# Kernel tuning notes

Hardware: AMD Instinct MI355X
Metric: run time of the kernel (lower is better)

The kernel has to match this reference:

```python
import jax, jax.numpy as jnp
import numpy as np

B, F, N, NO = 1, 512, 8192, 21
L1, L2, L3 = 640, 256, 128


def setup_inputs() -> dict:
    key = jax.random.key(0)
    ks = jax.random.split(key, 32)
    rn = lambda k, s: jax.random.normal(k, s, dtype=jnp.float32)
    inp = {
        "emb1": rn(ks[0], (B, F, N)),
        "emb2": rn(ks[1], (B, F, N)),
        "t1": rn(ks[2], (B, 3, N)),
        "t2": rn(ks[3], (B, 3, N)),
        "obj": jax.random.randint(ks[4], (B, 1), 0, NO, dtype=jnp.int32),
    }
    # 1x1 Conv1d weights == dense (out,in) matrices + bias
    dims_r = [(L1, 2 * F), (L2, L1), (L3, L2), (NO * 4, L3)]
    dims_t = [(L1, 2 * F), (L2, L1), (L3, L2), (NO * 3, L3)]
    ki = 5
    for br, dims in (("r", dims_r), ("t", dims_t)):
        for i, (o, c) in enumerate(dims, start=1):
            inp[f"w{i}{br}"] = rn(ks[ki], (o, c)) * (1.0 / np.sqrt(c)); ki += 1
            inp[f"b{i}{br}"] = rn(ks[ki], (o,)) * 0.01; ki += 1
    return inp


def _knn1(ref, qry):
    # ref, qry: (3, N). For each query point j, index of nearest ref point.
    g = ref.T @ qry  # (N_ref, N_qry)
    d2 = jnp.sum(ref * ref, axis=0)[:, None] + jnp.sum(qry * qry, axis=0)[None, :] - 2.0 * g
    return jnp.argmin(d2, axis=0)  # (N_qry,)


def _branch(x, w1, b1, w2, b2, w3, b3, w4, b4):
    h = jax.nn.relu(w1 @ x + b1[:, None])
    h = jax.nn.relu(w2 @ h + b2[:, None])
    h = jax.nn.relu(w3 @ h + b3[:, None])
    return w4 @ h + b4[:, None]


def reference(emb1, emb2, t1, t2, obj,
              w1r, b1r, w2r, b2r, w3r, b3r, w4r, b4r,
              w1t, b1t, w2t, b2t, w3t, b3t, w4t, b4t):
    bs, num_feat, num_points = emb1.shape
    t1 = t1.reshape(bs, 3, -1)
    t2 = t2.reshape(bs, 3, -1)
    # brute-force 1-NN of each t2 point among t1 points (bs == 1)
    idx = _knn1(t1[0], t2[0])  # (N,) zero-based (torch code subtracts 1 from 1-based inds)
    emb1g = emb1[0][:, idx]  # gather matched features, (F, N)
    # torch.stack([emb1,emb2],dim=1).view(bs, 2F, N) == channel concat [emb1g; emb2]
    emb = jnp.concatenate([emb1g, emb2[0]], axis=0)  # (2F, N)
    rx = _branch(emb, w1r, b1r, w2r, b2r, w3r, b3r, w4r, b4r).reshape(NO, 4, num_points)
    tx = _branch(emb, w1t, b1t, w2t, b2t, w3t, b3t, w4t, b4t).reshape(NO, 3, num_points)
    obj0 = obj[0]  # (1,)
    out_rx = jnp.transpose(rx[obj0], (0, 2, 1))  # (1, N, 4)
    out_tx = jnp.transpose(tx[obj0], (0, 2, 1))  # (1, N, 3)
    return out_rx, out_tx
```

## Files before the change

kernel.cpp:

```cpp
#include <hip/hip_runtime.h>

typedef unsigned short u16;
typedef __bf16 bf16x8 __attribute__((ext_vector_type(8)));
typedef float f32x4 __attribute__((ext_vector_type(4)));

__device__ __forceinline__ float b2f(u16 v) {
    return __uint_as_float(((unsigned int)v) << 16);
}
__device__ __forceinline__ u16 f2b(float f) {
    unsigned int u = __float_as_uint(f);
    u += 0x7fffu + ((u >> 16) & 1u);
    return (u16)(u >> 16);
}

__device__ __forceinline__ void ld_lds16(const u16* g, u16* l) {
    __builtin_amdgcn_global_load_lds(
        (__attribute__((address_space(1))) void*)(uintptr_t)(const void*)g,
        (__attribute__((address_space(3))) void*)l, 16, 0, 0);
}

__global__ void pack_w_k(const float* __restrict__ w1r, const float* __restrict__ w1t,
                         const float* __restrict__ w2r, const float* __restrict__ w2t,
                         const float* __restrict__ w3r, const float* __restrict__ w3t,
                         u16* __restrict__ dst)
{
    size_t i = (size_t)blockIdx.x * 2048 + (size_t)threadIdx.x * 8;
    const float* src; size_t off;
    if (i < 655360)       { src = w1r; off = 0; }
    else if (i < 1310720) { src = w1t; off = 655360; }
    else if (i < 1474560) { src = w2r; off = 1310720; }
    else if (i < 1638400) { src = w2t; off = 1474560; }
    else if (i < 1671168) { src = w3r; off = 1638400; }
    else                  { src = w3t; off = 1671168; }
    const float4 lo = *(const float4*)(src + (i - off));
    const float4 hi = *(const float4*)(src + (i - off) + 4);
    ushort4 o0, o1;
    o0.x = f2b(lo.x); o0.y = f2b(lo.y); o0.z = f2b(lo.z); o0.w = f2b(lo.w);
    o1.x = f2b(hi.x); o1.y = f2b(hi.y); o1.z = f2b(hi.z); o1.w = f2b(hi.w);
    *(ushort4*)(dst + i) = o0;
    *(ushort4*)(dst + i + 4) = o1;
}

__global__ void knn_k(const float* __restrict__ t1, const float* __restrict__ t2,
                      unsigned long long* __restrict__ keys)
{
    __shared__ float4 ref[128];
    const int t = threadIdx.x;
    const int rs = blockIdx.x;
    const int qb = blockIdx.y;
    if (t < 128) {
        int i = rs * 128 + t;
        float x = t1[i], y = t1[8192 + i], z = t1[16384 + i];
        float rr = __fadd_rn(__fadd_rn(__fmul_rn(x, x), __fmul_rn(y, y)), __fmul_rn(z, z));
        ref[t] = make_float4(x, y, z, rr);
    }
    __syncthreads();

    float qx[8], qy[8], qz[8], qq[8], bestd[8];
    int besti[8];
    const int q0 = qb * 2048 + t;
#pragma unroll
    for (int j = 0; j < 8; ++j) {
        int q = q0 + j * 256;
        qx[j] = t2[q]; qy[j] = t2[8192 + q]; qz[j] = t2[16384 + q];
        qq[j] = __fadd_rn(__fadd_rn(__fmul_rn(qx[j], qx[j]), __fmul_rn(qy[j], qy[j])),
                          __fmul_rn(qz[j], qz[j]));
        bestd[j] = __uint_as_float(0x7f800000u);
        besti[j] = 0;
    }
    for (int i = 0; i < 128; ++i) {
        float4 r = ref[i];
        int ridx = rs * 128 + i;
#pragma unroll
        for (int j = 0; j < 8; ++j) {
            float g = __fmaf_rn(qz[j], r.z, __fmaf_rn(qy[j], r.y, __fmul_rn(qx[j], r.x)));
            float d2 = __fsub_rn(__fadd_rn(r.w, qq[j]), __fmul_rn(2.0f, g));
            if (d2 < bestd[j]) { bestd[j] = d2; besti[j] = ridx; }
        }
    }
#pragma unroll
    for (int j = 0; j < 8; ++j) {
        unsigned long long key =
            ((unsigned long long)__float_as_uint(bestd[j]) << 32) | (unsigned int)besti[j];
        atomicMin(&keys[q0 + j * 256], key);
    }
}

__global__ void transpose_k(const float* __restrict__ e1, const float* __restrict__ e2,
                            u16* __restrict__ o1, u16* __restrict__ o2)
{
    __shared__ float tile[64][65];
    const float* in = blockIdx.z ? e2 : e1;
    u16* out = blockIdx.z ? o2 : o1;
    const int ostride = blockIdx.z ? 1024 : 512;
    const int coff = blockIdx.z ? 512 : 0;
    const int t = threadIdx.x;
    const int n0 = blockIdx.x * 64, f0 = blockIdx.y * 64;
    const int c = t & 63, r4 = t >> 6;
#pragma unroll
    for (int p = 0; p < 16; ++p) {
        int fr = p * 4 + r4;
        tile[fr][c] = in[(size_t)(f0 + fr) * 8192 + n0 + c];
    }
    __syncthreads();
    const int fc = (t & 15) * 4;
    const int nr4 = t >> 4;
#pragma unroll
    for (int p = 0; p < 4; ++p) {
        int nr = p * 16 + nr4;
        ushort4 o;
        o.x = f2b(tile[fc + 0][nr]); o.y = f2b(tile[fc + 1][nr]);
        o.z = f2b(tile[fc + 2][nr]); o.w = f2b(tile[fc + 3][nr]);
        *(ushort4*)&out[(size_t)(n0 + nr) * ostride + coff + f0 + fc] = o;
    }
}

__global__ void gather_k(const unsigned long long* __restrict__ keys,
                         const u16* __restrict__ emb1t, u16* __restrict__ Xt)
{
    const int t = threadIdx.x, w = t >> 6, l = t & 63;
    const int nbase = blockIdx.x * 32;
#pragma unroll
    for (int it = 0; it < 8; ++it) {
        int n = nbase + it * 4 + w;
        int i = (int)(keys[n] & 0xffffffffu);
        const uint4* src = (const uint4*)(emb1t + (size_t)i * 512);
        uint4* dst = (uint4*)(Xt + (size_t)n * 1024);
        dst[l] = src[l];
    }
}

template <int TN>
__global__ __launch_bounds__(256) void gemm_bt(
    const u16* __restrict__ Ar, const u16* __restrict__ At,
    const float* __restrict__ biasr, const float* __restrict__ biast,
    const u16* __restrict__ Bt, u16* __restrict__ Ct,
    int Mh, int K, int bstride, int b_step, int ostride, int relu)
{
    constexpr int NJ = TN / 32;
    __shared__ __align__(16) u16 lds_a[128 * 32];
    __shared__ __align__(16) u16 lds_b[TN * 32];

    const int t = threadIdx.x;
    const int n0 = blockIdx.x * TN;
    const int m0 = blockIdx.y * 128;
    const int branch = blockIdx.z;

    const u16* A = branch ? At : Ar;
    const float* bias = branch ? biast : biasr;
    const int b_off = branch * b_step;
    const int out_off = branch * Mh;

    const int w = t >> 6, l = t & 63;
    const int sr = l >> 2, sc = (l & 3) * 8;

    const u16* gA0 = A + (size_t)(m0 + w * 32 + sr) * K + sc;
    const u16* gA1 = gA0 + (size_t)16 * K;
    u16* lA0 = &lds_a[w * 1024];
    u16* lA1 = lA0 + 512;

    const u16* gB0;
    const u16* gB1 = nullptr;
    u16 *lB0, *lB1 = nullptr;
    if (TN == 128) {
        gB0 = Bt + (size_t)(n0 + w * 32 + sr) * bstride + b_off + sc;
        gB1 = gB0 + (size_t)16 * bstride;
        lB0 = &lds_b[w * 1024];
        lB1 = lB0 + 512;
    } else {
        gB0 = Bt + (size_t)(n0 + w * 16 + sr) * bstride + b_off + sc;
        lB0 = &lds_b[w * 512];
    }

    const int wm = (w & 1) * 64;
    const int wn = (w >> 1) * (TN / 2);
    const int lrow = l & 15, quad = l >> 4;
    const u16* fa = &lds_a[(wm + lrow) * 32 + quad * 8];
    const u16* fb = &lds_b[(wn + lrow) * 32 + quad * 8];

    f32x4 acc[4][NJ];
#pragma unroll
    for (int i = 0; i < 4; ++i)
#pragma unroll
        for (int j = 0; j < NJ; ++j)
            acc[i][j] = (f32x4){0.f, 0.f, 0.f, 0.f};

    ld_lds16(gA0, lA0); ld_lds16(gA1, lA1);
    ld_lds16(gB0, lB0);
    if (TN == 128) ld_lds16(gB1, lB1);

    for (int kt = 0; kt < K; kt += 32) {
        __syncthreads();
        bf16x8 af[4], bfr[NJ];
#pragma unroll
        for (int i = 0; i < 4; ++i) af[i] = *(const bf16x8*)(fa + i * 16 * 32);
#pragma unroll
        for (int j = 0; j < NJ; ++j) bfr[j] = *(const bf16x8*)(fb + j * 16 * 32);
        __syncthreads();
        if (kt + 32 < K) {
            gA0 += 32; gA1 += 32; gB0 += 32;
            ld_lds16(gA0, lA0); ld_lds16(gA1, lA1);
            ld_lds16(gB0, lB0);
            if (TN == 128) { gB1 += 32; ld_lds16(gB1, lB1); }
        }
#pragma unroll
        for (int i = 0; i < 4; ++i)
#pragma unroll
            for (int j = 0; j < NJ; ++j)
                acc[i][j] = __builtin_amdgcn_mfma_f32_16x16x32_bf16(
                    af[i], bfr[j], acc[i][j], 0, 0, 0);
    }

#pragma unroll
    for (int i = 0; i < 4; ++i) {
        const int mbase = m0 + wm + i * 16 + quad * 4;
        const float4 bbv = *(const float4*)&bias[mbase];
#pragma unroll
        for (int j = 0; j < NJ; ++j) {
            const int n = n0 + wn + j * 16 + lrow;
            f32x4 v = acc[i][j];
            float x0 = v[0] + bbv.x, x1 = v[1] + bbv.y;
            float x2 = v[2] + bbv.z, x3 = v[3] + bbv.w;
            if (relu) {
                x0 = fmaxf(x0, 0.f); x1 = fmaxf(x1, 0.f);
                x2 = fmaxf(x2, 0.f); x3 = fmaxf(x3, 0.f);
            }
            ushort4 o;
            o.x = f2b(x0); o.y = f2b(x1); o.z = f2b(x2); o.w = f2b(x3);
            *(ushort4*)&Ct[(size_t)n * ostride + out_off + mbase] = o;
        }
    }
}

__global__ __launch_bounds__(256) void gemm3_final_k(
    const u16* __restrict__ Ar, const u16* __restrict__ At,
    const float* __restrict__ b3r, const float* __restrict__ b3t,
    const u16* __restrict__ Bt,
    const float* __restrict__ w4r, const float* __restrict__ b4r,
    const float* __restrict__ w4t, const float* __restrict__ b4t,
    const int* __restrict__ objp, float* __restrict__ out)
{
    __shared__ __align__(16) u16 lds_a[128 * 32];
    __shared__ __align__(16) u16 lds_b[64 * 32];
    __shared__ __align__(16) float lds_h[64 * 132];
    __shared__ __align__(16) float lds_w[4 * 132];

    const int t = threadIdx.x;
    const int n0 = blockIdx.x * 64;
    const int branch = blockIdx.y;

    const u16* A = branch ? At : Ar;
    const float* bias = branch ? b3t : b3r;
    const int b_off = branch * 256;

    const int w = t >> 6, l = t & 63;
    const int sr = l >> 2, sc = (l & 3) * 8;

    const u16* gA0 = A + (size_t)(w * 32 + sr) * 256 + sc;
    const u16* gA1 = gA0 + (size_t)16 * 256;
    u16* lA0 = &lds_a[w * 1024];
    u16* lA1 = lA0 + 512;

    const u16* gB0 = Bt + (size_t)(n0 + w * 16 + sr) * 512 + b_off + sc;
    u16* lB0 = &lds_b[w * 512];

    const int wm = (w & 1) * 64;
    const int wn = (w >> 1) * 32;
    const int lrow = l & 15, quad = l >> 4;
    const u16* fa = &lds_a[(wm + lrow) * 32 + quad * 8];
    const u16* fb = &lds_b[(wn + lrow) * 32 + quad * 8];

    f32x4 acc[4][2];
#pragma unroll
    for (int i = 0; i < 4; ++i)
#pragma unroll
        for (int j = 0; j < 2; ++j)
            acc[i][j] = (f32x4){0.f, 0.f, 0.f, 0.f};

    ld_lds16(gA0, lA0); ld_lds16(gA1, lA1);
    ld_lds16(gB0, lB0);

    for (int kt = 0; kt < 256; kt += 32) {
        __syncthreads();
        bf16x8 af[4], bfr[2];
#pragma unroll
        for (int i = 0; i < 4; ++i) af[i] = *(const bf16x8*)(fa + i * 16 * 32);
#pragma unroll
        for (int j = 0; j < 2; ++j) bfr[j] = *(const bf16x8*)(fb + j * 16 * 32);
        __syncthreads();
        if (kt + 32 < 256) {
            gA0 += 32; gA1 += 32; gB0 += 32;
            ld_lds16(gA0, lA0); ld_lds16(gA1, lA1);
            ld_lds16(gB0, lB0);
        }
#pragma unroll
        for (int i = 0; i < 4; ++i)
#pragma unroll
            for (int j = 0; j < 2; ++j)
                acc[i][j] = __builtin_amdgcn_mfma_f32_16x16x32_bf16(
                    af[i], bfr[j], acc[i][j], 0, 0, 0);
    }

#pragma unroll
    for (int i = 0; i < 4; ++i) {
        const int mbase = wm + i * 16 + quad * 4;
        const float4 bbv = *(const float4*)&bias[mbase];
#pragma unroll
        for (int j = 0; j < 2; ++j) {
            const int nl = wn + j * 16 + lrow;
            f32x4 v = acc[i][j];
            float4 x;
            x.x = fmaxf(v[0] + bbv.x, 0.f); x.y = fmaxf(v[1] + bbv.y, 0.f);
            x.z = fmaxf(v[2] + bbv.z, 0.f); x.w = fmaxf(v[3] + bbv.w, 0.f);
            *(float4*)&lds_h[nl * 132 + mbase] = x;
        }
    }
    const int o = objp[0];
    const int NR = branch ? 3 : 4;
    const float* w4 = branch ? w4t : w4r;
    if (t < 128) {
        for (int r = 0; r < NR; ++r)
            lds_w[r * 132 + t] = w4[(size_t)(o * NR + r) * 128 + t];
    }
    __syncthreads();

    const int nl = t >> 2, k = t & 3;
    if (k < NR) {
        const float4* hp = (const float4*)&lds_h[nl * 132];
        const float4* wp4 = (const float4*)&lds_w[k * 132];
        float s = 0.f;
#pragma unroll
        for (int m4 = 0; m4 < 32; ++m4) {
            float4 h = hp[m4], ww = wp4[m4];
            s = fmaf(h.x, ww.x, s); s = fmaf(h.y, ww.y, s);
            s = fmaf(h.z, ww.z, s); s = fmaf(h.w, ww.w, s);
        }
        const int n = n0 + nl;
        if (branch == 0) out[(size_t)n * 4 + k] = s + b4r[o * 4 + k];
        else             out[32768 + (size_t)n * 3 + k] = s + b4t[o * 3 + k];
    }
}

extern "C" void kernel_launch(void* const* d_in, const int* in_sizes, int n_in,
                              void* d_out, int out_size, void* d_ws, size_t ws_size,
                              hipStream_t stream)
{
    const float* emb1 = (const float*)d_in[0];
    const float* emb2 = (const float*)d_in[1];
    const float* t1   = (const float*)d_in[2];
    const float* t2   = (const float*)d_in[3];
    const int*   obj  = (const int*)d_in[4];
    const float* w1r = (const float*)d_in[5];  const float* b1r = (const float*)d_in[6];
    const float* w2r = (const float*)d_in[7];  const float* b2r = (const float*)d_in[8];
    const float* w3r = (const float*)d_in[9];  const float* b3r = (const float*)d_in[10];
    const float* w4r = (const float*)d_in[11]; const float* b4r = (const float*)d_in[12];
    const float* w1t = (const float*)d_in[13]; const float* b1t = (const float*)d_in[14];
    const float* w2t = (const float*)d_in[15]; const float* b2t = (const float*)d_in[16];
    const float* w3t = (const float*)d_in[17]; const float* b3t = (const float*)d_in[18];
    const float* w4t = (const float*)d_in[19]; const float* b4t = (const float*)d_in[20];

    char* ws = (char*)d_ws;
    unsigned long long* keys = (unsigned long long*)ws;
    u16* emb1t = (u16*)(ws + (1u << 16));
    u16* Xt    = (u16*)(ws + (1u << 16) + (8u << 20));
    u16* h1t   = (u16*)(ws + (1u << 16) + (24u << 20));
    u16* wp    = (u16*)(ws + (1u << 16) + (44u << 20));
    u16* h2t   = emb1t;

    u16* w1rp = wp;            u16* w1tp = wp + 655360;
    u16* w2rp = wp + 1310720;  u16* w2tp = wp + 1474560;
    u16* w3rp = wp + 1638400;  u16* w3tp = wp + 1671168;

    hipMemsetAsync(keys, 0xFF, 8192 * sizeof(unsigned long long), stream);
    pack_w_k<<<832, 256, 0, stream>>>(w1r, w1t, w2r, w2t, w3r, w3t, wp);
    knn_k<<<dim3(64, 4), 256, 0, stream>>>(t1, t2, keys);
    transpose_k<<<dim3(128, 8, 2), 256, 0, stream>>>(emb1, emb2, emb1t, Xt);
    gather_k<<<256, 256, 0, stream>>>(keys, emb1t, Xt);
    gemm_bt<128><<<dim3(64, 5, 2), 256, 0, stream>>>(w1rp, w1tp, b1r, b1t, Xt,  h1t, 640, 1024, 1024,   0, 1280, 1);
    gemm_bt<64><<<dim3(128, 2, 2), 256, 0, stream>>>(w2rp, w2tp, b2r, b2t, h1t, h2t, 256,  640, 1280, 640,  512, 1);
    gemm3_final_k<<<dim3(128, 2), 256, 0, stream>>>(w3rp, w3tp, b3r, b3t, h2t,
                                                    w4r, b4r, w4t, b4t, obj, (float*)d_out);
}
```

Baseline: 201.9 us.

## Fuse prep kernels, replace atomic kNN with partial-reduce, gather inside GEMM1

Merges weight packing, the kNN partial search and the embedding transpose into one launch that dispatches on block index. This removes the memset and several launches and lets the independent stages run concurrently. The kNN now writes per-slice partial keys and a separate reduce kernel takes the min instead of using 64-bit atomics. The explicit gather kernel and the concatenated Xt buffer are removed: the first GEMM loads matched emb1 rows by index directly, then switches to emb2t halfway through K. This saves a full 16 MB write and read pass, at the cost of extra partial-key traffic and irregular row loads inside the GEMM.

```diff
diff --git a/kernel.cpp b/kernel.cpp
--- a/kernel.cpp
+++ b/kernel.cpp
@@ -1,6 +1,7 @@
 #include <hip/hip_runtime.h>
 
 typedef unsigned short u16;
+typedef unsigned long long u64;
 typedef __bf16 bf16x8 __attribute__((ext_vector_type(8)));
 typedef float f32x4 __attribute__((ext_vector_type(4)));
 
@@ -19,114 +20,219 @@
         (__attribute__((address_space(3))) void*)l, 16, 0, 0);
 }
 
-__global__ void pack_w_k(const float* __restrict__ w1r, const float* __restrict__ w1t,
-                         const float* __restrict__ w2r, const float* __restrict__ w2t,
-                         const float* __restrict__ w3r, const float* __restrict__ w3t,
-                         u16* __restrict__ dst)
-{
-    size_t i = (size_t)blockIdx.x * 2048 + (size_t)threadIdx.x * 8;
-    const float* src; size_t off;
-    if (i < 655360)       { src = w1r; off = 0; }
-    else if (i < 1310720) { src = w1t; off = 655360; }
-    else if (i < 1474560) { src = w2r; off = 1310720; }
-    else if (i < 1638400) { src = w2t; off = 1474560; }
-    else if (i < 1671168) { src = w3r; off = 1638400; }
-    else                  { src = w3t; off = 1671168; }
-    const float4 lo = *(const float4*)(src + (i - off));
-    const float4 hi = *(const float4*)(src + (i - off) + 4);
-    ushort4 o0, o1;
-    o0.x = f2b(lo.x); o0.y = f2b(lo.y); o0.z = f2b(lo.z); o0.w = f2b(lo.w);
-    o1.x = f2b(hi.x); o1.y = f2b(hi.y); o1.z = f2b(hi.z); o1.w = f2b(hi.w);
-    *(ushort4*)(dst + i) = o0;
-    *(ushort4*)(dst + i + 4) = o1;
-}
-
-__global__ void knn_k(const float* __restrict__ t1, const float* __restrict__ t2,
-                      unsigned long long* __restrict__ keys)
-{
-    __shared__ float4 ref[128];
+#define PREP_PACK_END  832
+#define PREP_KNN_END   1344
+#define PREP_TRANS_END 3392
+
+__global__ __launch_bounds__(256) void prep_k(
+    const float* __restrict__ w1r, const float* __restrict__ w1t,
+    const float* __restrict__ w2r, const float* __restrict__ w2t,
+    const float* __restrict__ w3r, const float* __restrict__ w3t,
+    u16* __restrict__ wdst,
+    const float* __restrict__ t1, const float* __restrict__ t2,
+    u64* __restrict__ part,
+    const float* __restrict__ e1, const float* __restrict__ e2,
+    u16* __restrict__ o1, u16* __restrict__ o2)
+{
+    __shared__ __align__(16) float smem[64 * 65];
+    const int bid = blockIdx.x;
     const int t = threadIdx.x;
-    const int rs = blockIdx.x;
-    const int qb = blockIdx.y;
-    if (t < 128) {
-        int i = rs * 128 + t;
-        float x = t1[i], y = t1[8192 + i], z = t1[16384 + i];
-        float rr = __fadd_rn(__fadd_rn(__fmul_rn(x, x), __fmul_rn(y, y)), __fmul_rn(z, z));
-        ref[t] = make_float4(x, y, z, rr);
-    }
-    __syncthreads();
-
-    float qx[8], qy[8], qz[8], qq[8], bestd[8];
-    int besti[8];
-    const int q0 = qb * 2048 + t;
-#pragma unroll
-    for (int j = 0; j < 8; ++j) {
-        int q = q0 + j * 256;
-        qx[j] = t2[q]; qy[j] = t2[8192 + q]; qz[j] = t2[16384 + q];
-        qq[j] = __fadd_rn(__fadd_rn(__fmul_rn(qx[j], qx[j]), __fmul_rn(qy[j], qy[j])),
-                          __fmul_rn(qz[j], qz[j]));
-        bestd[j] = __uint_as_float(0x7f800000u);
-        besti[j] = 0;
-    }
-    for (int i = 0; i < 128; ++i) {
-        float4 r = ref[i];
-        int ridx = rs * 128 + i;
-#pragma unroll
-        for (int j = 0; j < 8; ++j) {
-            float g = __fmaf_rn(qz[j], r.z, __fmaf_rn(qy[j], r.y, __fmul_rn(qx[j], r.x)));
-            float d2 = __fsub_rn(__fadd_rn(r.w, qq[j]), __fmul_rn(2.0f, g));
-            if (d2 < bestd[j]) { bestd[j] = d2; besti[j] = ridx; }
-        }
-    }
-#pragma unroll
-    for (int j = 0; j < 8; ++j) {
-        unsigned long long key =
-            ((unsigned long long)__float_as_uint(bestd[j]) << 32) | (unsigned int)besti[j];
-        atomicMin(&keys[q0 + j * 256], key);
-    }
-}
-
-__global__ void transpose_k(const float* __restrict__ e1, const float* __restrict__ e2,
-                            u16* __restrict__ o1, u16* __restrict__ o2)
-{
-    __shared__ float tile[64][65];
-    const float* in = blockIdx.z ? e2 : e1;
-    u16* out = blockIdx.z ? o2 : o1;
-    const int ostride = blockIdx.z ? 1024 : 512;
-    const int coff = blockIdx.z ? 512 : 0;
+
+    if (bid < PREP_PACK_END) {
+        size_t i = (size_t)bid * 2048 + (size_t)t * 8;
+        const float* src; size_t off;
+        if (i < 655360)       { src = w1r; off = 0; }
+        else if (i < 1310720) { src = w1t; off = 655360; }
+        else if (i < 1474560) { src = w2r; off = 1310720; }
+        else if (i < 1638400) { src = w2t; off = 1474560; }
+        else if (i < 1671168) { src = w3r; off = 1638400; }
+        else                  { src = w3t; off = 1671168; }
+        const float4 lo = *(const float4*)(src + (i - off));
+        const float4 hi = *(const float4*)(src + (i - off) + 4);
+        ushort4 o0v, o1v;
+        o0v.x = f2b(lo.x); o0v.y = f2b(lo.y); o0v.z = f2b(lo.z); o0v.w = f2b(lo.w);
+        o1v.x = f2b(hi.x); o1v.y = f2b(hi.y); o1v.z = f2b(hi.z); o1v.w = f2b(hi.w);
+        *(ushort4*)(wdst + i) = o0v;
+        *(ushort4*)(wdst + i + 4) = o1v;
+    } else if (bid < PREP_KNN_END) {
+        float4* ref = (float4*)smem;
+        const int rb = bid - PREP_PACK_END;
+        const int rs = rb & 63;
+        const int qb = rb >> 6;
+        if (t < 128) {
+            int i = rs * 128 + t;
+            float x = t1[i], y = t1[8192 + i], z = t1[16384 + i];
+            float rr = __fadd_rn(__fadd_rn(__fmul_rn(x, x), __fmul_rn(y, y)), __fmul_rn(z, z));
+            ref[t] = make_float4(x, y, z, rr);
+        }
+        __syncthreads();
+
+        float qx[4], qy[4], qz[4], qq[4], bestd[4];
+        int besti[4];
+        const int q0 = qb * 1024 + t;
+#pragma unroll
+        for (int j = 0; j < 4; ++j) {
+            int q = q0 + j * 256;
+            qx[j] = t2[q]; qy[j] = t2[8192 + q]; qz[j] = t2[16384 + q];
+            qq[j] = __fadd_rn(__fadd_rn(__fmul_rn(qx[j], qx[j]), __fmul_rn(qy[j], qy[j])),
+                              __fmul_rn(qz[j], qz[j]));
+            bestd[j] = __uint_as_float(0x7f800000u);
+            besti[j] = 0;
+        }
+        for (int i = 0; i < 128; ++i) {
+            float4 r = ref[i];
+            int ridx = rs * 128 + i;
+#pragma unroll
+            for (int j = 0; j < 4; ++j) {
+                float g = __fmaf_rn(qz[j], r.z, __fmaf_rn(qy[j], r.y, __fmul_rn(qx[j], r.x)));
+                float d2 = __fsub_rn(__fadd_rn(r.w, qq[j]), __fmul_rn(2.0f, g));
+                if (d2 < bestd[j]) { bestd[j] = d2; besti[j] = i + rs * 128; }
+            }
+        }
+#pragma unroll
+        for (int j = 0; j < 4; ++j) {
+            u64 key = ((u64)__float_as_uint(bestd[j]) << 32) | (unsigned int)besti[j];
+            part[(size_t)rs * 8192 + q0 + j * 256] = key;
+        }
+    } else {
+        float (*tile)[65] = (float(*)[65])smem;
+        const int tb = bid - PREP_KNN_END;
+        const int z = tb >> 10;
+        const int rem = tb & 1023;
+        const int fy = rem >> 7;
+        const int nx = rem & 127;
+        const float* in = z ? e2 : e1;
+        u16* out = z ? o2 : o1;
+        const int n0 = nx * 64, f0 = fy * 64;
+        const int c = t & 63, r4 = t >> 6;
+#pragma unroll
+        for (int p = 0; p < 16; ++p) {
+            int fr = p * 4 + r4;
+            tile[fr][c] = in[(size_t)(f0 + fr) * 8192 + n0 + c];
+        }
+        __syncthreads();
+        const int fc = (t & 15) * 4;
+        const int nr4 = t >> 4;
+#pragma unroll
+        for (int p = 0; p < 4; ++p) {
+            int nr = p * 16 + nr4;
+            ushort4 o;
+            o.x = f2b(tile[fc + 0][nr]); o.y = f2b(tile[fc + 1][nr]);
+            o.z = f2b(tile[fc + 2][nr]); o.w = f2b(tile[fc + 3][nr]);
+            *(ushort4*)&out[(size_t)(n0 + nr) * 512 + f0 + fc] = o;
+        }
+    }
+}
+
+__global__ __launch_bounds__(256) void knn_reduce_k(
+    const u64* __restrict__ part, unsigned int* __restrict__ idx)
+{
+    const int q = blockIdx.x * 256 + threadIdx.x;
+    u64 best = ~0ull;
+#pragma unroll
+    for (int s = 0; s < 64; ++s) {
+        u64 k = part[(size_t)s * 8192 + q];
+        best = k < best ? k : best;
+    }
+    idx[q] = (unsigned int)best;
+}
+
+__global__ __launch_bounds__(256) void gemm1_k(
+    const u16* __restrict__ Ar, const u16* __restrict__ At,
+    const float* __restrict__ biasr, const float* __restrict__ biast,
+    const u16* __restrict__ emb1t, const u16* __restrict__ emb2t,
+    const unsigned int* __restrict__ idx,
+    u16* __restrict__ Ct)
+{
+    constexpr int K = 1024;
+    __shared__ __align__(16) u16 lds_a[128 * 32];
+    __shared__ __align__(16) u16 lds_b[128 * 32];
+
     const int t = threadIdx.x;
-    const int n0 = blockIdx.x * 64, f0 = blockIdx.y * 64;
-    const int c = t & 63, r4 = t >> 6;
-#pragma unroll
-    for (int p = 0; p < 16; ++p) {
-        int fr = p * 4 + r4;
-        tile[fr][c] = in[(size_t)(f0 + fr) * 8192 + n0 + c];
-    }
-    __syncthreads();
-    const int fc = (t & 15) * 4;
-    const int nr4 = t >> 4;
-#pragma unroll
-    for (int p = 0; p < 4; ++p) {
-        int nr = p * 16 + nr4;
-        ushort4 o;
-        o.x = f2b(tile[fc + 0][nr]); o.y = f2b(tile[fc + 1][nr]);
-        o.z = f2b(tile[fc + 2][nr]); o.w = f2b(tile[fc + 3][nr]);
-        *(ushort4*)&out[(size_t)(n0 + nr) * ostride + coff + f0 + fc] = o;
-    }
-}
-
-__global__ void gather_k(const unsigned long long* __restrict__ keys,
-                         const u16* __restrict__ emb1t, u16* __restrict__ Xt)
-{
-    const int t = threadIdx.x, w = t >> 6, l = t & 63;
-    const int nbase = blockIdx.x * 32;
-#pragma unroll
-    for (int it = 0; it < 8; ++it) {
-        int n = nbase + it * 4 + w;
-        int i = (int)(keys[n] & 0xffffffffu);
-        const uint4* src = (const uint4*)(emb1t + (size_t)i * 512);
-        uint4* dst = (uint4*)(Xt + (size_t)n * 1024);
-        dst[l] = src[l];
+    const int n0 = blockIdx.x * 128;
+    const int m0 = blockIdx.y * 128;
+    const int branch = blockIdx.z;
+
+    const u16* A = branch ? At : Ar;
+    const float* bias = branch ? biast : biasr;
+    const int out_off = branch * 640;
+
+    const int w = t >> 6, l = t & 63;
+    const int sr = l >> 2, sc = (l & 3) * 8;
+
+    const u16* gA0 = A + (size_t)(m0 + w * 32 + sr) * K + sc;
+    const u16* gA1 = gA0 + (size_t)16 * K;
+    u16* lA0 = &lds_a[w * 1024];
+    u16* lA1 = lA0 + 512;
+
+    const int row0 = n0 + w * 32 + sr;
+    const int row1 = row0 + 16;
+    const unsigned int i0 = idx[row0];
+    const unsigned int i1 = idx[row1];
+    const u16* gB0 = emb1t + (size_t)i0 * 512 + sc;
+    const u16* gB1 = emb1t + (size_t)i1 * 512 + sc;
+    u16* lB0 = &lds_b[w * 1024];
+    u16* lB1 = lB0 + 512;
+
+    const int wm = (w & 1) * 64;
+    const int wn = (w >> 1) * 64;
+    const int lrow = l & 15, quad = l >> 4;
+    const u16* fa = &lds_a[(wm + lrow) * 32 + quad * 8];
+    const u16* fb = &lds_b[(wn + lrow) * 32 + quad * 8];
+
+    f32x4 acc[4][4];
+#pragma unroll
+    for (int i = 0; i < 4; ++i)
+#pragma unroll
+        for (int j = 0; j < 4; ++j)
+            acc[i][j] = (f32x4){0.f, 0.f, 0.f, 0.f};
+
+    ld_lds16(gA0, lA0); ld_lds16(gA1, lA1);
+    ld_lds16(gB0, lB0); ld_lds16(gB1, lB1);
+
+    for (int kt = 0; kt < K; kt += 32) {
+        __syncthreads();
+        bf16x8 af[4], bfr[4];
+#pragma unroll
+        for (int i = 0; i < 4; ++i) af[i] = *(const bf16x8*)(fa + i * 16 * 32);
+#pragma unroll
+        for (int j = 0; j < 4; ++j) bfr[j] = *(const bf16x8*)(fb + j * 16 * 32);
+        __syncthreads();
+        if (kt + 32 < K) {
+            gA0 += 32; gA1 += 32;
+            if (kt + 32 == 512) {
+                gB0 = emb2t + (size_t)row0 * 512 + sc;
+                gB1 = emb2t + (size_t)row1 * 512 + sc;
+            } else {
+                gB0 += 32; gB1 += 32;
+            }
+            ld_lds16(gA0, lA0); ld_lds16(gA1, lA1);
+            ld_lds16(gB0, lB0); ld_lds16(gB1, lB1);
+        }
+#pragma unroll
+        for (int i = 0; i < 4; ++i)
+#pragma unroll
+            for (int j = 0; j < 4; ++j)
+                acc[i][j] = __builtin_amdgcn_mfma_f32_16x16x32_bf16(
+                    af[i], bfr[j], acc[i][j], 0, 0, 0);
+    }
+
+#pragma unroll
+    for (int i = 0; i < 4; ++i) {
+        const int mbase = m0 + wm + i * 16 + quad * 4;
+        const float4 bbv = *(const float4*)&bias[mbase];
+#pragma unroll
+        for (int j = 0; j < 4; ++j) {
+            const int n = n0 + wn + j * 16 + lrow;
+            f32x4 v = acc[i][j];
+            float x0 = fmaxf(v[0] + bbv.x, 0.f);
+            float x1 = fmaxf(v[1] + bbv.y, 0.f);
+            float x2 = fmaxf(v[2] + bbv.z, 0.f);
+            float x3 = fmaxf(v[3] + bbv.w, 0.f);
+            ushort4 o;
+            o.x = f2b(x0); o.y = f2b(x1); o.z = f2b(x2); o.w = f2b(x3);
+            *(ushort4*)&Ct[(size_t)n * 1280 + out_off + mbase] = o;
+        }
     }
 }
 
@@ -360,24 +466,26 @@
     const float* w4t = (const float*)d_in[19]; const float* b4t = (const float*)d_in[20];
 
     char* ws = (char*)d_ws;
-    unsigned long long* keys = (unsigned long long*)ws;
-    u16* emb1t = (u16*)(ws + (1u << 16));
-    u16* Xt    = (u16*)(ws + (1u << 16) + (8u << 20));
-    u16* h1t   = (u16*)(ws + (1u << 16) + (24u << 20));
-    u16* wp    = (u16*)(ws + (1u << 16) + (44u << 20));
+    unsigned int* idx32 = (unsigned int*)ws;
+    u64* part  = (u64*)(ws + (1u << 16));
+    u16* emb1t = (u16*)(ws + (8u << 20));
+    u16* emb2t = (u16*)(ws + (16u << 20));
+    u16* h1t   = (u16*)(ws + (24u << 20));
+    u16* wp    = (u16*)(ws + (44u << 20));
     u16* h2t   = emb1t;
 
     u16* w1rp = wp;            u16* w1tp = wp + 655360;
     u16* w2rp = wp + 1310720;  u16* w2tp = wp + 1474560;
     u16* w3rp = wp + 1638400;  u16* w3tp = wp + 1671168;
 
-    hipMemsetAsync(keys, 0xFF, 8192 * sizeof(unsigned long long), stream);
-    pack_w_k<<<832, 256, 0, stream>>>(w1r, w1t, w2r, w2t, w3r, w3t, wp);
-    knn_k<<<dim3(64, 4), 256, 0, stream>>>(t1, t2, keys);
-    transpose_k<<<dim3(128, 8, 2), 256, 0, stream>>>(emb1, emb2, emb1t, Xt);
-    gather_k<<<256, 256, 0, stream>>>(keys, emb1t, Xt);
-    gemm_bt<128><<<dim3(64, 5, 2), 256, 0, stream>>>(w1rp, w1tp, b1r, b1t, Xt,  h1t, 640, 1024, 1024,   0, 1280, 1);
-    gemm_bt<64><<<dim3(128, 2, 2), 256, 0, stream>>>(w2rp, w2tp, b2r, b2t, h1t, h2t, 256,  640, 1280, 640,  512, 1);
+    prep_k<<<PREP_TRANS_END, 256, 0, stream>>>(w1r, w1t, w2r, w2t, w3r, w3t, wp,
+                                               t1, t2, part,
+                                               emb1, emb2, emb1t, emb2t);
+    knn_reduce_k<<<32, 256, 0, stream>>>(part, idx32);
+    gemm1_k<<<dim3(64, 5, 2), 256, 0, stream>>>(w1rp, w1tp, b1r, b1t,
+                                                emb1t, emb2t, idx32, h1t);
+    gemm_bt<64><<<dim3(128, 2, 2), 256, 0, stream>>>(w2rp, w2tp, b2r, b2t, h1t, h2t,
+                                                     256, 640, 1280, 640, 512, 1);
     gemm3_final_k<<<dim3(128, 2), 256, 0, stream>>>(w3rp, w3tp, b3r, b3t, h2t,
                                                     w4r, b4r, w4t, b4t, obj, (float*)d_out);
 }
```

New measurement: 187.9 us. 6.9% less time.
